# Kernel optimization log

Measured on AMD Instinct MI355X. Metric: run time of the kernel, lower is better.

## Reference

```python
import jax, jax.numpy as jnp
import numpy as np

HEADS = 8
EMBED = 64
FEAT_A = 256
FEAT_B = 256


def setup_inputs() -> dict:
    key = jax.random.key(0)
    k1, k2, k3, k4, k5 = jax.random.split(key, 5)
    B, N = 2, 2048
    z_a = jax.random.normal(k1, (B, FEAT_A, N), dtype=jnp.float32)
    z_b = jax.random.normal(k2, (B, FEAT_B, N), dtype=jnp.float32)
    # Conv1d(k=1, bias=False) weights, squeezed: [out_ch, in_ch]
    W_a = jax.random.normal(k3, (HEADS * EMBED, FEAT_A), dtype=jnp.float32) * (1.0 / np.sqrt(FEAT_A))
    W_b = jax.random.normal(k4, (HEADS * EMBED, FEAT_B), dtype=jnp.float32) * (1.0 / np.sqrt(FEAT_B))
    W_c = jax.random.normal(k5, (FEAT_A, HEADS * FEAT_B), dtype=jnp.float32) * (1.0 / np.sqrt(HEADS * FEAT_B))
    return {"z_a": z_a, "z_b": z_b, "W_a": W_a, "W_b": W_b, "W_c": W_c}


def reference(z_a, z_b, W_a, W_b, W_c):
    B, Fa, Na = z_a.shape
    Fb = z_b.shape[1]
    H, E = HEADS, EMBED
    norm = 1.0 / np.sqrt(E)
    # 1x1 conv embeddings -> q, k: [B, H, E, N]
    q = jnp.einsum('of,bfn->bon', W_a, z_a).reshape(B, H, E, Na)
    k = jnp.einsum('of,bfn->bon', W_b, z_b).reshape(B, H, E, -1)
    v = z_b  # [B, Fb, K]
    # coeff_pre_softmax[b,h,q,k] = (q^T k) / sqrt(E)
    pre = jnp.einsum('bheq,bhek->bhqk', q, k) * norm
    coeff = jax.nn.softmax(pre, axis=-1)  # softmax over keys (dim=2 in torch bmm form)
    # l1 loss: mean |pre| over (q,k) per head, averaged over heads
    l1 = jnp.mean(jnp.abs(pre), axis=(1, 2, 3))  # [B]
    # feat[b,h,q,f] = coeff @ v^T
    feat = jnp.einsum('bhqk,bfk->bhqf', coeff, v)
    # combine heads: w[h] = W_c[:, h*Fb:(h+1)*Fb].T  -> [H, Fb, Fa]
    w = W_c.reshape(Fa, H, Fb).transpose(1, 2, 0)
    out = jnp.einsum('bhqf,hfo->bqo', feat, w)  # sum over heads
    return out, l1
```

## Files before the change

### kernel.cpp

```cpp
#include <hip/hip_runtime.h>
#include <hip/hip_bf16.h>


#define B_ 2
#define N_ 2048
#define F_ 256
#define H_ 8
#define E_ 64

typedef __attribute__((ext_vector_type(8))) short bf16x8;
typedef __attribute__((ext_vector_type(4))) float f32x4;

__device__ __forceinline__ unsigned short f2b(float x) {
  __hip_bfloat16 h = __float2bfloat16(x);
  return *reinterpret_cast<unsigned short*>(&h);
}

__device__ __forceinline__ unsigned short f2bt(float x) {
  union { float f; unsigned u; } c; c.f = x;
  return (unsigned short)(c.u >> 16);
}

__device__ __forceinline__ f32x4 mfma16(bf16x8 a, bf16x8 b, f32x4 c) {
  return __builtin_amdgcn_mfma_f32_16x16x32_bf16(a, b, c, 0, 0, 0);
}

__device__ __forceinline__ void async_lds16(const unsigned short* g, unsigned short* l) {
  __builtin_amdgcn_global_load_lds(
      (const __attribute__((address_space(1))) unsigned int*)g,
      (__attribute__((address_space(3))) unsigned int*)l, 16, 0, 0);
}

__global__ __launch_bounds__(256) void prep_kernel(
    const float* __restrict__ z_b, unsigned short* __restrict__ vbf,
    const float* __restrict__ W_c, unsigned short* __restrict__ wcb,
    const float* __restrict__ W_a, const float* __restrict__ W_b,
    unsigned short* __restrict__ wab, float* __restrict__ l1acc) {
  int i = blockIdx.x * 256 + threadIdx.x;
  if (i < B_) l1acc[i] = 0.f;
  const int nzb = B_ * F_ * N_ / 4;
  const int nwc = F_ * H_ * F_ / 4;
  const int nw = 512 * F_ / 4;
  const float* src; unsigned short* dst; int j;
  if (i < nzb) { src = z_b; dst = vbf; j = i; }
  else if (i < nzb + nwc) { src = W_c; dst = wcb; j = i - nzb; }
  else if (i < nzb + nwc + nw) { src = W_a; dst = wab; j = i - nzb - nwc; }
  else { j = i - nzb - nwc - nw; if (j >= nw) return; src = W_b; dst = wab + 512 * F_; }
  float4 v = reinterpret_cast<const float4*>(src)[j];
  unsigned long long pk =
      ((unsigned long long)f2b(v.w) << 48) | ((unsigned long long)f2b(v.z) << 32) |
      ((unsigned long long)f2b(v.y) << 16) | (unsigned long long)f2b(v.x);
  reinterpret_cast<unsigned long long*>(dst)[j] = pk;
}

__global__ __launch_bounds__(256) void transp_kernel(
    const float* __restrict__ z_a, const float* __restrict__ z_b,
    unsigned short* __restrict__ zaT, unsigned short* __restrict__ zbT) {
  __shared__ unsigned int t32[64][65];
  const int tid = threadIdx.x;
  const int nt = blockIdx.x, ft = blockIdx.y, wz = blockIdx.z;
  const int b = wz & 1, which = wz >> 1;
  const float* src = (which ? z_b : z_a) + (size_t)b * F_ * N_;
  unsigned short* dst = (which ? zbT : zaT) + (size_t)b * N_ * F_;
  const int col = tid & 63, rb = tid >> 6;
#pragma unroll
  for (int i = 0; i < 16; ++i) {
    int row = rb + i * 4;
    t32[row][col] = f2b(src[(size_t)(ft * 64 + row) * N_ + nt * 64 + col]);
  }
  __syncthreads();
#pragma unroll
  for (int i = 0; i < 16; ++i) {
    int row = rb + i * 4;
    dst[(size_t)(nt * 64 + row) * F_ + ft * 64 + col] = (unsigned short)t32[col][row];
  }
}

__global__ __launch_bounds__(256) void proj_mfma(
    const unsigned short* __restrict__ zaT, const unsigned short* __restrict__ zbT,
    const unsigned short* __restrict__ wab,
    unsigned short* __restrict__ qT, unsigned short* __restrict__ kT) {
  __shared__ __align__(16) unsigned short As[2][64][32];
  __shared__ __align__(16) unsigned short Bs[2][64][32];

  const int tid = threadIdx.x;
  const int wid = tid >> 6, lane = tid & 63;
  const int quad = lane >> 4, l16 = lane & 15;
  const int nt = blockIdx.x, ot = blockIdx.y, wz = blockIdx.z;
  const int b = wz & 1, which = wz >> 1;

  const unsigned short* zsrc = (which ? zbT : zaT) + (size_t)b * N_ * F_;
  const unsigned short* wsrc = wab + (size_t)which * 512 * F_;
  unsigned short* dst = (which ? kT : qT) + (size_t)b * N_ * 512;
  const float scale = which ? 1.f : 0.125f;

  const int srow = wid * 16 + (lane >> 2);
  const int schunk = (lane & 3) ^ ((srow >> 1) & 3);
  const unsigned short* agl = zsrc + (size_t)(nt * 64 + srow) * F_ + schunk * 8;
  const unsigned short* bgl = wsrc + (size_t)(ot * 64 + srow) * F_ + schunk * 8;
  const int roff = (quad ^ ((l16 >> 1) & 3)) * 8;

  f32x4 acc[4];
  const f32x4 zero4 = {0.f, 0.f, 0.f, 0.f};
#pragma unroll
  for (int g = 0; g < 4; ++g) acc[g] = zero4;

  async_lds16(agl, &As[0][wid * 16][0]);
  async_lds16(bgl, &Bs[0][wid * 16][0]);
  __syncthreads();

#pragma unroll
  for (int kt = 0; kt < 8; ++kt) {
    const int cur = kt & 1;
    if (kt + 1 < 8) {
      async_lds16(agl + (kt + 1) * 32, &As[cur ^ 1][wid * 16][0]);
      async_lds16(bgl + (kt + 1) * 32, &Bs[cur ^ 1][wid * 16][0]);
    }
    bf16x8 bf = *reinterpret_cast<const bf16x8*>(&Bs[cur][0][0] + (wid * 16 + l16) * 32 + roff);
#pragma unroll
    for (int g = 0; g < 4; ++g) {
      bf16x8 af = *reinterpret_cast<const bf16x8*>(&As[cur][0][0] + (g * 16 + l16) * 32 + roff);
      acc[g] = mfma16(af, bf, acc[g]);
    }
    __syncthreads();
  }

#pragma unroll
  for (int g = 0; g < 4; ++g)
#pragma unroll
    for (int r = 0; r < 4; ++r)
      dst[(size_t)(nt * 64 + g * 16 + quad * 4 + r) * 512 + ot * 64 + wid * 16 + l16] =
          f2b(acc[g][r] * scale);
}

__global__ __launch_bounds__(256, 3) void attn_mfma(
    const unsigned short* __restrict__ qT, const unsigned short* __restrict__ kT,
    const unsigned short* __restrict__ vbf, unsigned short* __restrict__ feat,
    float* __restrict__ l1acc) {
  __shared__ __align__(16) unsigned short ks[2][32][64];
  __shared__ __align__(16) unsigned short vs[2][256][32];
  __shared__ __align__(16) unsigned short p_blk[2][64][40];
  __shared__ float lsum_sh[64];
  __shared__ float redblk[256];

  const int tid = threadIdx.x;
  const int wid = tid >> 6, lane = tid & 63;
  const int quad = lane >> 4, l16 = lane & 15;
  const int qt = blockIdx.x, h = blockIdx.y, b = blockIdx.z;

  const int kkey = wid * 8 + (lane >> 3);
  const int kchunk = (lane & 7) ^ ((kkey >> 1) & 7);
  const unsigned short* kgl =
      kT + ((size_t)(b * N_ + kkey) * 512) + h * 64 + kchunk * 8;
  const unsigned short* vgl[4];
#pragma unroll
  for (int j = 0; j < 4; ++j) {
    int f = (wid * 4 + j) * 16 + (lane >> 2);
    int c = (lane & 3) ^ ((f >> 1) & 3);
    vgl[j] = vbf + ((size_t)(b * F_ + f) * 2048) + c * 8;
  }

  const unsigned short* qrow =
      qT + (size_t)(b * N_ + qt * 64 + wid * 16 + l16) * 512 + h * 64 + quad * 8;
  bf16x8 qf0 = *reinterpret_cast<const bf16x8*>(qrow);
  bf16x8 qf1 = *reinterpret_cast<const bf16x8*>(qrow + 32);

  const int koff = ((quad ^ (l16 & 7)) * 8);
  const int voff = ((quad ^ ((l16 >> 1) & 3)) * 8);

  f32x4 acc[4][4];
  const f32x4 zero4 = {0.f, 0.f, 0.f, 0.f};
#pragma unroll
  for (int g = 0; g < 4; ++g)
#pragma unroll
    for (int t = 0; t < 4; ++t) acc[g][t] = zero4;
  float lsum[4] = {0.f, 0.f, 0.f, 0.f};
  float suml1 = 0.f;
  bf16x8 vreg[4];

  async_lds16(kgl, &ks[0][wid * 8][0]);
#pragma unroll
  for (int j = 0; j < 4; ++j) async_lds16(vgl[j], &vs[0][(wid * 4 + j) * 16][0]);
  __syncthreads();

#pragma unroll 2
  for (int kt = 0; kt < N_ / 32; ++kt) {
    const int cur = kt & 1;
    if (kt + 1 < N_ / 32) {
      async_lds16(kgl + (size_t)(kt + 1) * 32 * 512, &ks[cur ^ 1][wid * 8][0]);
#pragma unroll
      for (int j = 0; j < 4; ++j)
        async_lds16(vgl[j] + (kt + 1) * 32, &vs[cur ^ 1][(wid * 4 + j) * 16][0]);
    }

    const unsigned short* ksc = &ks[cur][0][0];
    bf16x8 kf00 = *reinterpret_cast<const bf16x8*>(ksc + (2 * l16) * 64 + koff);
    bf16x8 kf01 = *reinterpret_cast<const bf16x8*>(ksc + (2 * l16) * 64 + (koff ^ 32));
    bf16x8 kf10 = *reinterpret_cast<const bf16x8*>(ksc + (2 * l16 + 1) * 64 + koff);
    bf16x8 kf11 = *reinterpret_cast<const bf16x8*>(ksc + (2 * l16 + 1) * 64 + (koff ^ 32));

    f32x4 s0 = mfma16(qf0, kf00, zero4); s0 = mfma16(qf1, kf01, s0);
    f32x4 s1 = mfma16(qf0, kf10, zero4); s1 = mfma16(qf1, kf11, s1);

#pragma unroll
    for (int r = 0; r < 4; ++r) {
      float a0 = s0[r], a1 = s1[r];
      suml1 += fabsf(a0) + fabsf(a1);
      float p0 = __expf(a0), p1 = __expf(a1);
      lsum[r] += p0 + p1;
      unsigned pk = ((unsigned)f2bt(p1) << 16) | f2bt(p0);
      *reinterpret_cast<unsigned*>(&p_blk[cur][wid * 16 + quad * 4 + r][2 * l16]) = pk;
    }

    if (kt > 0) {
#pragma unroll
      for (int g = 0; g < 4; ++g) {
        bf16x8 pf = *reinterpret_cast<const bf16x8*>(&p_blk[cur ^ 1][g * 16 + l16][quad * 8]);
#pragma unroll
        for (int t = 0; t < 4; ++t) acc[g][t] = mfma16(pf, vreg[t], acc[g][t]);
      }
    }

    {
      const unsigned short* vsc = &vs[cur][0][0];
#pragma unroll
      for (int t = 0; t < 4; ++t) {
        int f = wid * 64 + t * 16 + l16;
        vreg[t] = *reinterpret_cast<const bf16x8*>(vsc + f * 32 + voff);
      }
    }
    __syncthreads();
  }

  {
#pragma unroll
    for (int g = 0; g < 4; ++g) {
      bf16x8 pf = *reinterpret_cast<const bf16x8*>(&p_blk[1][g * 16 + l16][quad * 8]);
#pragma unroll
      for (int t = 0; t < 4; ++t) acc[g][t] = mfma16(pf, vreg[t], acc[g][t]);
    }
  }

#pragma unroll
  for (int r = 0; r < 4; ++r) {
    float rs = lsum[r];
    rs += __shfl_xor(rs, 1);
    rs += __shfl_xor(rs, 2);
    rs += __shfl_xor(rs, 4);
    rs += __shfl_xor(rs, 8);
    if (l16 == 0) lsum_sh[wid * 16 + quad * 4 + r] = rs;
  }
  __syncthreads();

#pragma unroll
  for (int g = 0; g < 4; ++g)
#pragma unroll
    for (int r = 0; r < 4; ++r) {
      float invl = 1.f / lsum_sh[g * 16 + quad * 4 + r];
      unsigned short* fr =
          feat + (size_t)(b * N_ + qt * 64 + g * 16 + quad * 4 + r) * 2048 +
          h * 256 + wid * 64 + l16;
#pragma unroll
      for (int t = 0; t < 4; ++t) fr[t * 16] = f2b(acc[g][t][r] * invl);
    }

  redblk[tid] = suml1;
  __syncthreads();
  for (int st = 128; st > 0; st >>= 1) {
    if (tid < st) redblk[tid] += redblk[tid + st];
    __syncthreads();
  }
  if (tid == 0) atomicAdd(&l1acc[b], redblk[0]);
}

__global__ __launch_bounds__(256) void combine_mfma(
    const unsigned short* __restrict__ feat, const unsigned short* __restrict__ wcb,
    const float* __restrict__ l1acc, float* __restrict__ out) {
  __shared__ __align__(16) unsigned short As[2][64][32];
  __shared__ __align__(16) unsigned short Bs[2][32][32];

  const int tid = threadIdx.x;
  const int wid = tid >> 6, lane = tid & 63;
  const int quad = lane >> 4, l16 = lane & 15;
  const int mb = blockIdx.x, ob = blockIdx.y;
  const int ow = wid & 1, mh = wid >> 1;

  const int srow = wid * 16 + (lane >> 2);
  const int schunk = (lane & 3) ^ ((srow >> 1) & 3);
  const unsigned short* agl = feat + (size_t)(mb * 64 + srow) * 2048 + schunk * 8;
  const unsigned short* bgl = wcb + (size_t)(ob * 32 + srow) * 2048 + schunk * 8;

  const int roff = (quad ^ ((l16 >> 1) & 3)) * 8;

  f32x4 acc[2];
  const f32x4 zero4 = {0.f, 0.f, 0.f, 0.f};
#pragma unroll
  for (int g = 0; g < 2; ++g) acc[g] = zero4;

  async_lds16(agl, &As[0][wid * 16][0]);
  if (wid < 2) async_lds16(bgl, &Bs[0][wid * 16][0]);
  __syncthreads();

#pragma unroll 2
  for (int kt = 0; kt < 64; ++kt) {
    const int cur = kt & 1;
    if (kt + 1 < 64) {
      async_lds16(agl + (kt + 1) * 32, &As[cur ^ 1][wid * 16][0]);
      if (wid < 2) async_lds16(bgl + (kt + 1) * 32, &Bs[cur ^ 1][wid * 16][0]);
    }
    bf16x8 bf = *reinterpret_cast<const bf16x8*>(&Bs[cur][0][0] + (ow * 16 + l16) * 32 + roff);
#pragma unroll
    for (int g = 0; g < 2; ++g) {
      bf16x8 af =
          *reinterpret_cast<const bf16x8*>(&As[cur][0][0] + (mh * 32 + g * 16 + l16) * 32 + roff);
      acc[g] = mfma16(af, bf, acc[g]);
    }
    __syncthreads();
  }

#pragma unroll
  for (int g = 0; g < 2; ++g)
#pragma unroll
    for (int r = 0; r < 4; ++r)
      out[(size_t)(mb * 64 + mh * 32 + g * 16 + quad * 4 + r) * 256 +
          ob * 32 + ow * 16 + l16] = acc[g][r];

  if (mb == 0 && ob == 0 && tid < B_)
    out[(size_t)B_ * N_ * F_ + tid] = l1acc[tid] * (1.f / (float)(H_ * N_ * N_));
}

extern "C" void kernel_launch(void* const* d_in, const int* in_sizes, int n_in,
                              void* d_out, int out_size, void* d_ws, size_t ws_size,
                              hipStream_t stream) {
  const float* z_a = (const float*)d_in[0];
  const float* z_b = (const float*)d_in[1];
  const float* W_a = (const float*)d_in[2];
  const float* W_b = (const float*)d_in[3];
  const float* W_c = (const float*)d_in[4];
  float* out = (float*)d_out;

  char* ws = (char*)d_ws;
  unsigned short* qT = (unsigned short*)ws;
  unsigned short* kT = (unsigned short*)(ws + ((size_t)4 << 20));
  unsigned short* vbf = (unsigned short*)(ws + ((size_t)8 << 20));
  unsigned short* wcb = (unsigned short*)(ws + ((size_t)10 << 20));
  unsigned short* feat = (unsigned short*)(ws + ((size_t)11 << 20));
  float* l1acc = (float*)(ws + ((size_t)27 << 20));
  unsigned short* zaT = (unsigned short*)(ws + ((size_t)28 << 20));
  unsigned short* zbT = (unsigned short*)(ws + ((size_t)30 << 20));
  unsigned short* wab = (unsigned short*)(ws + ((size_t)32 << 20));

  const int nprep = B_ * F_ * N_ / 4 + F_ * H_ * F_ / 4 + 2 * (512 * F_ / 4);
  prep_kernel<<<dim3((nprep + 255) / 256), 256, 0, stream>>>(
      z_b, vbf, W_c, wcb, W_a, W_b, wab, l1acc);
  transp_kernel<<<dim3(N_ / 64, F_ / 64, 4), 256, 0, stream>>>(z_a, z_b, zaT, zbT);
  proj_mfma<<<dim3(N_ / 64, 8, 4), 256, 0, stream>>>(zaT, zbT, wab, qT, kT);
  attn_mfma<<<dim3(N_ / 64, H_, B_), 256, 0, stream>>>(qT, kT, vbf, feat, l1acc);
  combine_mfma<<<dim3(B_ * N_ / 64, 8), 256, 0, stream>>>(feat, wcb, l1acc, out);
}
```

Measured before the change: 167.7 us.

## Load K/V and GEMM operands directly from global into registers, bypassing LDS

The attention kernel stops staging K and V tiles through shared memory with async copies. Each lane now loads its MFMA fragments straight from global memory into double-buffered registers, and the launch-bounds occupancy hint is dropped. The combine GEMM gets the same treatment and loses its LDS tiles and per-iteration barrier. This removes LDS traffic and synchronisation, but each wave now fetches K and V separately, so data reuse across waves is lost and global and L2 traffic rises. V in particular is loaded with no prefetch distance.

Measured after the change: 245.3 us. +46.3%, slower.

```diff
diff --git a/kernel.cpp b/kernel.cpp
--- a/kernel.cpp
+++ b/kernel.cpp
@@ -133,12 +133,10 @@
           f2b(acc[g][r] * scale);
 }
 
-__global__ __launch_bounds__(256, 3) void attn_mfma(
+__global__ __launch_bounds__(256) void attn_mfma(
     const unsigned short* __restrict__ qT, const unsigned short* __restrict__ kT,
     const unsigned short* __restrict__ vbf, unsigned short* __restrict__ feat,
     float* __restrict__ l1acc) {
-  __shared__ __align__(16) unsigned short ks[2][32][64];
-  __shared__ __align__(16) unsigned short vs[2][256][32];
   __shared__ __align__(16) unsigned short p_blk[2][64][40];
   __shared__ float lsum_sh[64];
   __shared__ float redblk[256];
@@ -148,16 +146,16 @@
   const int quad = lane >> 4, l16 = lane & 15;
   const int qt = blockIdx.x, h = blockIdx.y, b = blockIdx.z;
 
-  const int kkey = wid * 8 + (lane >> 3);
-  const int kchunk = (lane & 7) ^ ((kkey >> 1) & 7);
-  const unsigned short* kgl =
-      kT + ((size_t)(b * N_ + kkey) * 512) + h * 64 + kchunk * 8;
-  const unsigned short* vgl[4];
-#pragma unroll
-  for (int j = 0; j < 4; ++j) {
-    int f = (wid * 4 + j) * 16 + (lane >> 2);
-    int c = (lane & 3) ^ ((f >> 1) & 3);
-    vgl[j] = vbf + ((size_t)(b * F_ + f) * 2048) + c * 8;
+  const unsigned short* kbase = kT + (size_t)b * N_ * 512 + h * 64;
+  const unsigned short* k00 = kbase + (size_t)(2 * l16) * 512 + quad * 8;
+  const unsigned short* k01 = k00 + 32;
+  const unsigned short* k10 = kbase + (size_t)(2 * l16 + 1) * 512 + quad * 8;
+  const unsigned short* k11 = k10 + 32;
+  const unsigned short* vp[4];
+#pragma unroll
+  for (int t = 0; t < 4; ++t) {
+    int f = wid * 64 + t * 16 + l16;
+    vp[t] = vbf + (size_t)(b * F_ + f) * 2048 + quad * 8;
   }
 
   const unsigned short* qrow =
@@ -165,9 +163,6 @@
   bf16x8 qf0 = *reinterpret_cast<const bf16x8*>(qrow);
   bf16x8 qf1 = *reinterpret_cast<const bf16x8*>(qrow + 32);
 
-  const int koff = ((quad ^ (l16 & 7)) * 8);
-  const int voff = ((quad ^ ((l16 >> 1) & 3)) * 8);
-
   f32x4 acc[4][4];
   const f32x4 zero4 = {0.f, 0.f, 0.f, 0.f};
 #pragma unroll
@@ -176,31 +171,30 @@
     for (int t = 0; t < 4; ++t) acc[g][t] = zero4;
   float lsum[4] = {0.f, 0.f, 0.f, 0.f};
   float suml1 = 0.f;
-  bf16x8 vreg[4];
-
-  async_lds16(kgl, &ks[0][wid * 8][0]);
-#pragma unroll
-  for (int j = 0; j < 4; ++j) async_lds16(vgl[j], &vs[0][(wid * 4 + j) * 16][0]);
-  __syncthreads();
+
+  bf16x8 kreg[2][4], vreg[2][4];
+  kreg[0][0] = *reinterpret_cast<const bf16x8*>(k00);
+  kreg[0][1] = *reinterpret_cast<const bf16x8*>(k01);
+  kreg[0][2] = *reinterpret_cast<const bf16x8*>(k10);
+  kreg[0][3] = *reinterpret_cast<const bf16x8*>(k11);
 
 #pragma unroll 2
   for (int kt = 0; kt < N_ / 32; ++kt) {
-    const int cur = kt & 1;
+    const int ph = kt & 1;
+
     if (kt + 1 < N_ / 32) {
-      async_lds16(kgl + (size_t)(kt + 1) * 32 * 512, &ks[cur ^ 1][wid * 8][0]);
-#pragma unroll
-      for (int j = 0; j < 4; ++j)
-        async_lds16(vgl[j] + (kt + 1) * 32, &vs[cur ^ 1][(wid * 4 + j) * 16][0]);
-    }
-
-    const unsigned short* ksc = &ks[cur][0][0];
-    bf16x8 kf00 = *reinterpret_cast<const bf16x8*>(ksc + (2 * l16) * 64 + koff);
-    bf16x8 kf01 = *reinterpret_cast<const bf16x8*>(ksc + (2 * l16) * 64 + (koff ^ 32));
-    bf16x8 kf10 = *reinterpret_cast<const bf16x8*>(ksc + (2 * l16 + 1) * 64 + koff);
-    bf16x8 kf11 = *reinterpret_cast<const bf16x8*>(ksc + (2 * l16 + 1) * 64 + (koff ^ 32));
-
-    f32x4 s0 = mfma16(qf0, kf00, zero4); s0 = mfma16(qf1, kf01, s0);
-    f32x4 s1 = mfma16(qf0, kf10, zero4); s1 = mfma16(qf1, kf11, s1);
+      const size_t ko = (size_t)(kt + 1) * 32 * 512;
+      kreg[ph ^ 1][0] = *reinterpret_cast<const bf16x8*>(k00 + ko);
+      kreg[ph ^ 1][1] = *reinterpret_cast<const bf16x8*>(k01 + ko);
+      kreg[ph ^ 1][2] = *reinterpret_cast<const bf16x8*>(k10 + ko);
+      kreg[ph ^ 1][3] = *reinterpret_cast<const bf16x8*>(k11 + ko);
+    }
+#pragma unroll
+    for (int t = 0; t < 4; ++t)
+      vreg[ph][t] = *reinterpret_cast<const bf16x8*>(vp[t] + kt * 32);
+
+    f32x4 s0 = mfma16(qf0, kreg[ph][0], zero4); s0 = mfma16(qf1, kreg[ph][1], s0);
+    f32x4 s1 = mfma16(qf0, kreg[ph][2], zero4); s1 = mfma16(qf1, kreg[ph][3], s1);
 
 #pragma unroll
     for (int r = 0; r < 4; ++r) {
@@ -209,24 +203,15 @@
       float p0 = __expf(a0), p1 = __expf(a1);
       lsum[r] += p0 + p1;
       unsigned pk = ((unsigned)f2bt(p1) << 16) | f2bt(p0);
-      *reinterpret_cast<unsigned*>(&p_blk[cur][wid * 16 + quad * 4 + r][2 * l16]) = pk;
+      *reinterpret_cast<unsigned*>(&p_blk[ph][wid * 16 + quad * 4 + r][2 * l16]) = pk;
     }
 
     if (kt > 0) {
 #pragma unroll
       for (int g = 0; g < 4; ++g) {
-        bf16x8 pf = *reinterpret_cast<const bf16x8*>(&p_blk[cur ^ 1][g * 16 + l16][quad * 8]);
-#pragma unroll
-        for (int t = 0; t < 4; ++t) acc[g][t] = mfma16(pf, vreg[t], acc[g][t]);
-      }
-    }
-
-    {
-      const unsigned short* vsc = &vs[cur][0][0];
-#pragma unroll
-      for (int t = 0; t < 4; ++t) {
-        int f = wid * 64 + t * 16 + l16;
-        vreg[t] = *reinterpret_cast<const bf16x8*>(vsc + f * 32 + voff);
+        bf16x8 pf = *reinterpret_cast<const bf16x8*>(&p_blk[ph ^ 1][g * 16 + l16][quad * 8]);
+#pragma unroll
+        for (int t = 0; t < 4; ++t) acc[g][t] = mfma16(pf, vreg[ph ^ 1][t], acc[g][t]);
       }
     }
     __syncthreads();
@@ -237,7 +222,7 @@
     for (int g = 0; g < 4; ++g) {
       bf16x8 pf = *reinterpret_cast<const bf16x8*>(&p_blk[1][g * 16 + l16][quad * 8]);
 #pragma unroll
-      for (int t = 0; t < 4; ++t) acc[g][t] = mfma16(pf, vreg[t], acc[g][t]);
+      for (int t = 0; t < 4; ++t) acc[g][t] = mfma16(pf, vreg[1][t], acc[g][t]);
     }
   }
 
@@ -276,46 +261,37 @@
 __global__ __launch_bounds__(256) void combine_mfma(
     const unsigned short* __restrict__ feat, const unsigned short* __restrict__ wcb,
     const float* __restrict__ l1acc, float* __restrict__ out) {
-  __shared__ __align__(16) unsigned short As[2][64][32];
-  __shared__ __align__(16) unsigned short Bs[2][32][32];
-
   const int tid = threadIdx.x;
   const int wid = tid >> 6, lane = tid & 63;
   const int quad = lane >> 4, l16 = lane & 15;
   const int mb = blockIdx.x, ob = blockIdx.y;
   const int ow = wid & 1, mh = wid >> 1;
 
-  const int srow = wid * 16 + (lane >> 2);
-  const int schunk = (lane & 3) ^ ((srow >> 1) & 3);
-  const unsigned short* agl = feat + (size_t)(mb * 64 + srow) * 2048 + schunk * 8;
-  const unsigned short* bgl = wcb + (size_t)(ob * 32 + srow) * 2048 + schunk * 8;
-
-  const int roff = (quad ^ ((l16 >> 1) & 3)) * 8;
+  const unsigned short* a0p =
+      feat + (size_t)(mb * 64 + mh * 32 + l16) * 2048 + quad * 8;
+  const unsigned short* a1p = a0p + (size_t)16 * 2048;
+  const unsigned short* bp =
+      wcb + (size_t)(ob * 32 + ow * 16 + l16) * 2048 + quad * 8;
 
   f32x4 acc[2];
   const f32x4 zero4 = {0.f, 0.f, 0.f, 0.f};
-#pragma unroll
-  for (int g = 0; g < 2; ++g) acc[g] = zero4;
-
-  async_lds16(agl, &As[0][wid * 16][0]);
-  if (wid < 2) async_lds16(bgl, &Bs[0][wid * 16][0]);
-  __syncthreads();
+  acc[0] = zero4; acc[1] = zero4;
+
+  bf16x8 ar[2][2], br[2];
+  ar[0][0] = *reinterpret_cast<const bf16x8*>(a0p);
+  ar[0][1] = *reinterpret_cast<const bf16x8*>(a1p);
+  br[0] = *reinterpret_cast<const bf16x8*>(bp);
 
 #pragma unroll 2
   for (int kt = 0; kt < 64; ++kt) {
-    const int cur = kt & 1;
+    const int ph = kt & 1;
     if (kt + 1 < 64) {
-      async_lds16(agl + (kt + 1) * 32, &As[cur ^ 1][wid * 16][0]);
-      if (wid < 2) async_lds16(bgl + (kt + 1) * 32, &Bs[cur ^ 1][wid * 16][0]);
-    }
-    bf16x8 bf = *reinterpret_cast<const bf16x8*>(&Bs[cur][0][0] + (ow * 16 + l16) * 32 + roff);
-#pragma unroll
-    for (int g = 0; g < 2; ++g) {
-      bf16x8 af =
-          *reinterpret_cast<const bf16x8*>(&As[cur][0][0] + (mh * 32 + g * 16 + l16) * 32 + roff);
-      acc[g] = mfma16(af, bf, acc[g]);
-    }
-    __syncthreads();
+      ar[ph ^ 1][0] = *reinterpret_cast<const bf16x8*>(a0p + (kt + 1) * 32);
+      ar[ph ^ 1][1] = *reinterpret_cast<const bf16x8*>(a1p + (kt + 1) * 32);
+      br[ph ^ 1] = *reinterpret_cast<const bf16x8*>(bp + (kt + 1) * 32);
+    }
+    acc[0] = mfma16(ar[ph][0], br[ph], acc[0]);
+    acc[1] = mfma16(ar[ph][1], br[ph], acc[1]);
   }
 
 #pragma unroll
```

## Split attention over key halves and merge partial results in a separate kernel

Applied to the files above, without the earlier changes.

Templates the attention kernel so each block can process half of the keys, doubling the grid from 512 to 1024 blocks. Per-half unnormalized outputs and row sums go to workspace, and a new merge kernel adds the halves and applies the softmax normalization. The aim is better occupancy and latency hiding on the many CUs of the GPU. In exchange it adds an extra kernel launch, extra global traffic for the partial feature buffers, and an extra bf16 rounding step. V register fragments are also double-buffered by iteration parity. The split path only runs if the workspace is at least 48MB, otherwise the unsplit path still pays for the merge pass.

New measurement: 180.5 us. +7.7%, slower.

```diff
diff --git a/kernel.cpp b/kernel.cpp
--- a/kernel.cpp
+++ b/kernel.cpp
@@ -19,6 +19,11 @@
 __device__ __forceinline__ unsigned short f2bt(float x) {
   union { float f; unsigned u; } c; c.f = x;
   return (unsigned short)(c.u >> 16);
+}
+
+__device__ __forceinline__ float b2f(unsigned short u) {
+  union { unsigned u; float f; } c; c.u = (unsigned)u << 16;
+  return c.f;
 }
 
 __device__ __forceinline__ f32x4 mfma16(bf16x8 a, bf16x8 b, f32x4 c) {
@@ -133,31 +138,35 @@
           f2b(acc[g][r] * scale);
 }
 
+template <int S>
 __global__ __launch_bounds__(256, 3) void attn_mfma(
     const unsigned short* __restrict__ qT, const unsigned short* __restrict__ kT,
-    const unsigned short* __restrict__ vbf, unsigned short* __restrict__ feat,
-    float* __restrict__ l1acc) {
+    const unsigned short* __restrict__ vbf, unsigned short* __restrict__ featp,
+    float* __restrict__ lpart, float* __restrict__ l1acc) {
   __shared__ __align__(16) unsigned short ks[2][32][64];
   __shared__ __align__(16) unsigned short vs[2][256][32];
   __shared__ __align__(16) unsigned short p_blk[2][64][40];
-  __shared__ float lsum_sh[64];
   __shared__ float redblk[256];
 
+  const int NITER = 64 >> S;
   const int tid = threadIdx.x;
   const int wid = tid >> 6, lane = tid & 63;
   const int quad = lane >> 4, l16 = lane & 15;
-  const int qt = blockIdx.x, h = blockIdx.y, b = blockIdx.z;
+  const int qt = blockIdx.x, h = blockIdx.y;
+  const int half = blockIdx.z & ((1 << S) - 1);
+  const int b = blockIdx.z >> S;
+  const int key0 = half * (NITER * 32);
 
   const int kkey = wid * 8 + (lane >> 3);
   const int kchunk = (lane & 7) ^ ((kkey >> 1) & 7);
   const unsigned short* kgl =
-      kT + ((size_t)(b * N_ + kkey) * 512) + h * 64 + kchunk * 8;
+      kT + ((size_t)(b * N_ + key0 + kkey) * 512) + h * 64 + kchunk * 8;
   const unsigned short* vgl[4];
 #pragma unroll
   for (int j = 0; j < 4; ++j) {
     int f = (wid * 4 + j) * 16 + (lane >> 2);
     int c = (lane & 3) ^ ((f >> 1) & 3);
-    vgl[j] = vbf + ((size_t)(b * F_ + f) * 2048) + c * 8;
+    vgl[j] = vbf + ((size_t)(b * F_ + f) * 2048) + key0 + c * 8;
   }
 
   const unsigned short* qrow =
@@ -176,7 +185,7 @@
     for (int t = 0; t < 4; ++t) acc[g][t] = zero4;
   float lsum[4] = {0.f, 0.f, 0.f, 0.f};
   float suml1 = 0.f;
-  bf16x8 vreg[4];
+  bf16x8 vreg[2][4];
 
   async_lds16(kgl, &ks[0][wid * 8][0]);
 #pragma unroll
@@ -184,9 +193,9 @@
   __syncthreads();
 
 #pragma unroll 2
-  for (int kt = 0; kt < N_ / 32; ++kt) {
+  for (int kt = 0; kt < NITER; ++kt) {
     const int cur = kt & 1;
-    if (kt + 1 < N_ / 32) {
+    if (kt + 1 < NITER) {
       async_lds16(kgl + (size_t)(kt + 1) * 32 * 512, &ks[cur ^ 1][wid * 8][0]);
 #pragma unroll
       for (int j = 0; j < 4; ++j)
@@ -217,7 +226,7 @@
       for (int g = 0; g < 4; ++g) {
         bf16x8 pf = *reinterpret_cast<const bf16x8*>(&p_blk[cur ^ 1][g * 16 + l16][quad * 8]);
 #pragma unroll
-        for (int t = 0; t < 4; ++t) acc[g][t] = mfma16(pf, vreg[t], acc[g][t]);
+        for (int t = 0; t < 4; ++t) acc[g][t] = mfma16(pf, vreg[cur ^ 1][t], acc[g][t]);
       }
     }
 
@@ -226,7 +235,7 @@
 #pragma unroll
       for (int t = 0; t < 4; ++t) {
         int f = wid * 64 + t * 16 + l16;
-        vreg[t] = *reinterpret_cast<const bf16x8*>(vsc + f * 32 + voff);
+        vreg[cur][t] = *reinterpret_cast<const bf16x8*>(vsc + f * 32 + voff);
       }
     }
     __syncthreads();
@@ -237,7 +246,7 @@
     for (int g = 0; g < 4; ++g) {
       bf16x8 pf = *reinterpret_cast<const bf16x8*>(&p_blk[1][g * 16 + l16][quad * 8]);
 #pragma unroll
-      for (int t = 0; t < 4; ++t) acc[g][t] = mfma16(pf, vreg[t], acc[g][t]);
+      for (int t = 0; t < 4; ++t) acc[g][t] = mfma16(pf, vreg[1][t], acc[g][t]);
     }
   }
 
@@ -248,20 +257,19 @@
     rs += __shfl_xor(rs, 2);
     rs += __shfl_xor(rs, 4);
     rs += __shfl_xor(rs, 8);
-    if (l16 == 0) lsum_sh[wid * 16 + quad * 4 + r] = rs;
-  }
-  __syncthreads();
+    if (l16 == 0)
+      lpart[(((size_t)half * B_ + b) * H_ + h) * N_ + qt * 64 + wid * 16 + quad * 4 + r] = rs;
+  }
 
 #pragma unroll
   for (int g = 0; g < 4; ++g)
 #pragma unroll
     for (int r = 0; r < 4; ++r) {
-      float invl = 1.f / lsum_sh[g * 16 + quad * 4 + r];
       unsigned short* fr =
-          feat + (size_t)(b * N_ + qt * 64 + g * 16 + quad * 4 + r) * 2048 +
+          featp + ((size_t)(half * B_ + b) * N_ + qt * 64 + g * 16 + quad * 4 + r) * 2048 +
           h * 256 + wid * 64 + l16;
 #pragma unroll
-      for (int t = 0; t < 4; ++t) fr[t * 16] = f2b(acc[g][t][r] * invl);
+      for (int t = 0; t < 4; ++t) fr[t * 16] = f2b(acc[g][t][r]);
     }
 
   redblk[tid] = suml1;
@@ -273,6 +281,30 @@
   if (tid == 0) atomicAdd(&l1acc[b], redblk[0]);
 }
 
+__global__ __launch_bounds__(256) void merge_kernel(
+    unsigned short* __restrict__ f0, const unsigned short* __restrict__ f1,
+    const float* __restrict__ lpart, int nsplit) {
+  const int n = blockIdx.x, b = blockIdx.y, t = threadIdx.x;
+  const int o0 = t * 8, h = o0 >> 8;
+  const size_t lidx = ((size_t)b * H_ + h) * N_ + n;
+  float l = lpart[lidx];
+  if (nsplit == 2) l += lpart[(size_t)B_ * H_ * N_ + lidx];
+  const float linv = 1.f / l;
+  const size_t idx = ((size_t)b * N_ + n) * 2048 + o0;
+  bf16x8 a = *reinterpret_cast<const bf16x8*>(f0 + idx);
+  unsigned short r[8];
+  if (nsplit == 2) {
+    bf16x8 c = *reinterpret_cast<const bf16x8*>(f1 + (size_t)B_ * N_ * 2048 + idx);
+#pragma unroll
+    for (int j = 0; j < 8; ++j)
+      r[j] = f2b((b2f((unsigned short)a[j]) + b2f((unsigned short)c[j])) * linv);
+  } else {
+#pragma unroll
+    for (int j = 0; j < 8; ++j) r[j] = f2b(b2f((unsigned short)a[j]) * linv);
+  }
+  *reinterpret_cast<bf16x8*>(f0 + idx) = *reinterpret_cast<bf16x8*>(r);
+}
+
 __global__ __launch_bounds__(256) void combine_mfma(
     const unsigned short* __restrict__ feat, const unsigned short* __restrict__ wcb,
     const float* __restrict__ l1acc, float* __restrict__ out) {
@@ -294,8 +326,7 @@
 
   f32x4 acc[2];
   const f32x4 zero4 = {0.f, 0.f, 0.f, 0.f};
-#pragma unroll
-  for (int g = 0; g < 2; ++g) acc[g] = zero4;
+  acc[0] = zero4; acc[1] = zero4;
 
   async_lds16(agl, &As[0][wid * 16][0]);
   if (wid < 2) async_lds16(bgl, &Bs[0][wid * 16][0]);
@@ -344,17 +375,28 @@
   unsigned short* kT = (unsigned short*)(ws + ((size_t)4 << 20));
   unsigned short* vbf = (unsigned short*)(ws + ((size_t)8 << 20));
   unsigned short* wcb = (unsigned short*)(ws + ((size_t)10 << 20));
-  unsigned short* feat = (unsigned short*)(ws + ((size_t)11 << 20));
-  float* l1acc = (float*)(ws + ((size_t)27 << 20));
-  unsigned short* zaT = (unsigned short*)(ws + ((size_t)28 << 20));
-  unsigned short* zbT = (unsigned short*)(ws + ((size_t)30 << 20));
-  unsigned short* wab = (unsigned short*)(ws + ((size_t)32 << 20));
+  unsigned short* zaT = (unsigned short*)(ws + ((size_t)11 << 20));
+  unsigned short* zbT = (unsigned short*)(ws + ((size_t)13 << 20));
+  unsigned short* wab = (unsigned short*)(ws + ((size_t)15 << 20));
+  float* lpart = (float*)(ws + ((size_t)15 << 20) + (512 << 10));
+  float* l1acc = (float*)(ws + ((size_t)15 << 20) + (768 << 10));
+  unsigned short* featp = (unsigned short*)(ws + ((size_t)16 << 20));
+
+  const bool split = ws_size >= ((size_t)48 << 20);
 
   const int nprep = B_ * F_ * N_ / 4 + F_ * H_ * F_ / 4 + 2 * (512 * F_ / 4);
   prep_kernel<<<dim3((nprep + 255) / 256), 256, 0, stream>>>(
       z_b, vbf, W_c, wcb, W_a, W_b, wab, l1acc);
   transp_kernel<<<dim3(N_ / 64, F_ / 64, 4), 256, 0, stream>>>(z_a, z_b, zaT, zbT);
   proj_mfma<<<dim3(N_ / 64, 8, 4), 256, 0, stream>>>(zaT, zbT, wab, qT, kT);
-  attn_mfma<<<dim3(N_ / 64, H_, B_), 256, 0, stream>>>(qT, kT, vbf, feat, l1acc);
-  combine_mfma<<<dim3(B_ * N_ / 64, 8), 256, 0, stream>>>(feat, wcb, l1acc, out);
-}
+  if (split) {
+    attn_mfma<1><<<dim3(N_ / 64, H_, B_ * 2), 256, 0, stream>>>(
+        qT, kT, vbf, featp, lpart, l1acc);
+    merge_kernel<<<dim3(N_, B_), 256, 0, stream>>>(featp, featp, lpart, 2);
+  } else {
+    attn_mfma<0><<<dim3(N_ / 64, H_, B_), 256, 0, stream>>>(
+        qT, kT, vbf, featp, lpart, l1acc);
+    merge_kernel<<<dim3(N_, B_), 256, 0, stream>>>(featp, featp, lpart, 1);
+  }
+  combine_mfma<<<dim3(B_ * N_ / 64, 8), 256, 0, stream>>>(featp, wcb, l1acc, out);
+}
```

## Process 128 queries per attention block to reuse K/V tiles

Applied to the files above, without the earlier changes.

The attention kernel now gives each wave two 16-row query fragments, so a block covers 128 queries instead of 64. Every K and V tile loaded into shared memory then serves twice as many score and PV MFMAs, and the grid along N is halved. The V register fragments are double-buffered by iteration parity, and the workspace offsets are rearranged. The costs are many more accumulator registers per thread (launch bound relaxed from 3 to 2 blocks per CU) and only 256 blocks in the grid, which cuts occupancy and the latency hiding that comes with it.

Result: slower. 174.9 us (+4.3%).

```diff
diff --git a/kernel.cpp b/kernel.cpp
--- a/kernel.cpp
+++ b/kernel.cpp
@@ -133,14 +133,14 @@
           f2b(acc[g][r] * scale);
 }
 
-__global__ __launch_bounds__(256, 3) void attn_mfma(
+__global__ __launch_bounds__(256, 2) void attn_mfma(
     const unsigned short* __restrict__ qT, const unsigned short* __restrict__ kT,
     const unsigned short* __restrict__ vbf, unsigned short* __restrict__ feat,
     float* __restrict__ l1acc) {
   __shared__ __align__(16) unsigned short ks[2][32][64];
   __shared__ __align__(16) unsigned short vs[2][256][32];
-  __shared__ __align__(16) unsigned short p_blk[2][64][40];
-  __shared__ float lsum_sh[64];
+  __shared__ __align__(16) unsigned short p_blk[2][128][40];
+  __shared__ float lsum_sh[128];
   __shared__ float redblk[256];
 
   const int tid = threadIdx.x;
@@ -160,23 +160,25 @@
     vgl[j] = vbf + ((size_t)(b * F_ + f) * 2048) + c * 8;
   }
 
-  const unsigned short* qrow =
-      qT + (size_t)(b * N_ + qt * 64 + wid * 16 + l16) * 512 + h * 64 + quad * 8;
-  bf16x8 qf0 = *reinterpret_cast<const bf16x8*>(qrow);
-  bf16x8 qf1 = *reinterpret_cast<const bf16x8*>(qrow + 32);
+  const unsigned short* qrowA =
+      qT + (size_t)(b * N_ + qt * 128 + wid * 32 + l16) * 512 + h * 64 + quad * 8;
+  bf16x8 qA0 = *reinterpret_cast<const bf16x8*>(qrowA);
+  bf16x8 qA1 = *reinterpret_cast<const bf16x8*>(qrowA + 32);
+  bf16x8 qB0 = *reinterpret_cast<const bf16x8*>(qrowA + (size_t)16 * 512);
+  bf16x8 qB1 = *reinterpret_cast<const bf16x8*>(qrowA + (size_t)16 * 512 + 32);
 
   const int koff = ((quad ^ (l16 & 7)) * 8);
   const int voff = ((quad ^ ((l16 >> 1) & 3)) * 8);
 
-  f32x4 acc[4][4];
+  f32x4 acc[8][4];
   const f32x4 zero4 = {0.f, 0.f, 0.f, 0.f};
 #pragma unroll
-  for (int g = 0; g < 4; ++g)
+  for (int g = 0; g < 8; ++g)
 #pragma unroll
     for (int t = 0; t < 4; ++t) acc[g][t] = zero4;
-  float lsum[4] = {0.f, 0.f, 0.f, 0.f};
+  float lsum[8] = {0.f, 0.f, 0.f, 0.f, 0.f, 0.f, 0.f, 0.f};
   float suml1 = 0.f;
-  bf16x8 vreg[4];
+  bf16x8 vreg[2][4];
 
   async_lds16(kgl, &ks[0][wid * 8][0]);
 #pragma unroll
@@ -199,25 +201,33 @@
     bf16x8 kf10 = *reinterpret_cast<const bf16x8*>(ksc + (2 * l16 + 1) * 64 + koff);
     bf16x8 kf11 = *reinterpret_cast<const bf16x8*>(ksc + (2 * l16 + 1) * 64 + (koff ^ 32));
 
-    f32x4 s0 = mfma16(qf0, kf00, zero4); s0 = mfma16(qf1, kf01, s0);
-    f32x4 s1 = mfma16(qf0, kf10, zero4); s1 = mfma16(qf1, kf11, s1);
+    f32x4 sA0 = mfma16(qA0, kf00, zero4); sA0 = mfma16(qA1, kf01, sA0);
+    f32x4 sA1 = mfma16(qA0, kf10, zero4); sA1 = mfma16(qA1, kf11, sA1);
+    f32x4 sB0 = mfma16(qB0, kf00, zero4); sB0 = mfma16(qB1, kf01, sB0);
+    f32x4 sB1 = mfma16(qB0, kf10, zero4); sB1 = mfma16(qB1, kf11, sB1);
 
 #pragma unroll
     for (int r = 0; r < 4; ++r) {
-      float a0 = s0[r], a1 = s1[r];
+      float a0 = sA0[r], a1 = sA1[r];
       suml1 += fabsf(a0) + fabsf(a1);
       float p0 = __expf(a0), p1 = __expf(a1);
       lsum[r] += p0 + p1;
       unsigned pk = ((unsigned)f2bt(p1) << 16) | f2bt(p0);
-      *reinterpret_cast<unsigned*>(&p_blk[cur][wid * 16 + quad * 4 + r][2 * l16]) = pk;
+      *reinterpret_cast<unsigned*>(&p_blk[cur][wid * 32 + quad * 4 + r][2 * l16]) = pk;
+      float b0 = sB0[r], b1 = sB1[r];
+      suml1 += fabsf(b0) + fabsf(b1);
+      float p2 = __expf(b0), p3 = __expf(b1);
+      lsum[4 + r] += p2 + p3;
+      unsigned pk2 = ((unsigned)f2bt(p3) << 16) | f2bt(p2);
+      *reinterpret_cast<unsigned*>(&p_blk[cur][wid * 32 + 16 + quad * 4 + r][2 * l16]) = pk2;
     }
 
     if (kt > 0) {
 #pragma unroll
-      for (int g = 0; g < 4; ++g) {
+      for (int g = 0; g < 8; ++g) {
         bf16x8 pf = *reinterpret_cast<const bf16x8*>(&p_blk[cur ^ 1][g * 16 + l16][quad * 8]);
 #pragma unroll
-        for (int t = 0; t < 4; ++t) acc[g][t] = mfma16(pf, vreg[t], acc[g][t]);
+        for (int t = 0; t < 4; ++t) acc[g][t] = mfma16(pf, vreg[cur ^ 1][t], acc[g][t]);
       }
     }
 
@@ -226,7 +236,7 @@
 #pragma unroll
       for (int t = 0; t < 4; ++t) {
         int f = wid * 64 + t * 16 + l16;
-        vreg[t] = *reinterpret_cast<const bf16x8*>(vsc + f * 32 + voff);
+        vreg[cur][t] = *reinterpret_cast<const bf16x8*>(vsc + f * 32 + voff);
       }
     }
     __syncthreads();
@@ -234,31 +244,32 @@
 
   {
 #pragma unroll
-    for (int g = 0; g < 4; ++g) {
+    for (int g = 0; g < 8; ++g) {
       bf16x8 pf = *reinterpret_cast<const bf16x8*>(&p_blk[1][g * 16 + l16][quad * 8]);
 #pragma unroll
-      for (int t = 0; t < 4; ++t) acc[g][t] = mfma16(pf, vreg[t], acc[g][t]);
-    }
-  }
-
-#pragma unroll
-  for (int r = 0; r < 4; ++r) {
+      for (int t = 0; t < 4; ++t) acc[g][t] = mfma16(pf, vreg[1][t], acc[g][t]);
+    }
+  }
+
+#pragma unroll
+  for (int r = 0; r < 8; ++r) {
     float rs = lsum[r];
     rs += __shfl_xor(rs, 1);
     rs += __shfl_xor(rs, 2);
     rs += __shfl_xor(rs, 4);
     rs += __shfl_xor(rs, 8);
-    if (l16 == 0) lsum_sh[wid * 16 + quad * 4 + r] = rs;
-  }
-  __syncthreads();
-
-#pragma unroll
-  for (int g = 0; g < 4; ++g)
+    if (l16 == 0)
+      lsum_sh[wid * 32 + (r >> 2) * 16 + quad * 4 + (r & 3)] = rs;
+  }
+  __syncthreads();
+
+#pragma unroll
+  for (int g = 0; g < 8; ++g)
 #pragma unroll
     for (int r = 0; r < 4; ++r) {
       float invl = 1.f / lsum_sh[g * 16 + quad * 4 + r];
       unsigned short* fr =
-          feat + (size_t)(b * N_ + qt * 64 + g * 16 + quad * 4 + r) * 2048 +
+          feat + (size_t)(b * N_ + qt * 128 + g * 16 + quad * 4 + r) * 2048 +
           h * 256 + wid * 64 + l16;
 #pragma unroll
       for (int t = 0; t < 4; ++t) fr[t * 16] = f2b(acc[g][t][r] * invl);
@@ -294,8 +305,7 @@
 
   f32x4 acc[2];
   const f32x4 zero4 = {0.f, 0.f, 0.f, 0.f};
-#pragma unroll
-  for (int g = 0; g < 2; ++g) acc[g] = zero4;
+  acc[0] = zero4; acc[1] = zero4;
 
   async_lds16(agl, &As[0][wid * 16][0]);
   if (wid < 2) async_lds16(bgl, &Bs[0][wid * 16][0]);
@@ -344,17 +354,17 @@
   unsigned short* kT = (unsigned short*)(ws + ((size_t)4 << 20));
   unsigned short* vbf = (unsigned short*)(ws + ((size_t)8 << 20));
   unsigned short* wcb = (unsigned short*)(ws + ((size_t)10 << 20));
-  unsigned short* feat = (unsigned short*)(ws + ((size_t)11 << 20));
-  float* l1acc = (float*)(ws + ((size_t)27 << 20));
-  unsigned short* zaT = (unsigned short*)(ws + ((size_t)28 << 20));
-  unsigned short* zbT = (unsigned short*)(ws + ((size_t)30 << 20));
-  unsigned short* wab = (unsigned short*)(ws + ((size_t)32 << 20));
+  unsigned short* zaT = (unsigned short*)(ws + ((size_t)11 << 20));
+  unsigned short* zbT = (unsigned short*)(ws + ((size_t)13 << 20));
+  unsigned short* wab = (unsigned short*)(ws + ((size_t)15 << 20));
+  float* l1acc = (float*)(ws + ((size_t)15 << 20) + (768 << 10));
+  unsigned short* feat = (unsigned short*)(ws + ((size_t)16 << 20));
 
   const int nprep = B_ * F_ * N_ / 4 + F_ * H_ * F_ / 4 + 2 * (512 * F_ / 4);
   prep_kernel<<<dim3((nprep + 255) / 256), 256, 0, stream>>>(
       z_b, vbf, W_c, wcb, W_a, W_b, wab, l1acc);
   transp_kernel<<<dim3(N_ / 64, F_ / 64, 4), 256, 0, stream>>>(z_a, z_b, zaT, zbT);
   proj_mfma<<<dim3(N_ / 64, 8, 4), 256, 0, stream>>>(zaT, zbT, wab, qT, kT);
-  attn_mfma<<<dim3(N_ / 64, H_, B_), 256, 0, stream>>>(qT, kT, vbf, feat, l1acc);
+  attn_mfma<<<dim3(N_ / 128, H_, B_), 256, 0, stream>>>(qT, kT, vbf, feat, l1acc);
   combine_mfma<<<dim3(B_ * N_ / 64, 8), 256, 0, stream>>>(feat, wcb, l1acc, out);
 }
```
